# Kernel optimization log

Measured on AMD Instinct MI355X. Metric: run time of the kernel, lower is better.

The kernel has to match this reference:

```python
import jax, jax.numpy as jnp
import numpy as np

N, E, R = 50000, 1600000, 8
IN_F, HID_F, OUT_F = 128, 64, 64


def setup_inputs() -> dict:
    key = jax.random.key(0)
    ks = jax.random.split(key, 9)
    x = jax.random.normal(ks[0], (N, IN_F), dtype=jnp.float32)
    edge_index = jax.random.randint(ks[1], (2, E), 0, N, dtype=jnp.int64)
    edge_type = jax.random.randint(ks[2], (E,), 0, R, dtype=jnp.int64)
    # layer 1 params (scaled like glorot)
    s1 = 1.0 / np.sqrt(IN_F)
    W1_rel = jax.random.normal(ks[3], (R, IN_F, HID_F), dtype=jnp.float32) * s1
    W1_root = jax.random.normal(ks[4], (IN_F, HID_F), dtype=jnp.float32) * s1
    b1 = jnp.zeros((HID_F,), dtype=jnp.float32)
    # layer 2 params
    s2 = 1.0 / np.sqrt(HID_F)
    W2_rel = jax.random.normal(ks[5], (R, HID_F, OUT_F), dtype=jnp.float32) * s2
    W2_root = jax.random.normal(ks[6], (HID_F, OUT_F), dtype=jnp.float32) * s2
    b2 = jnp.zeros((OUT_F,), dtype=jnp.float32)
    return {"x": x, "edge_index": edge_index, "edge_type": edge_type,
            "W1_rel": W1_rel, "W1_root": W1_root, "b1": b1,
            "W2_rel": W2_rel, "W2_root": W2_root, "b2": b2}


def _rgcn_conv(x, src, dst, etype, W_rel, W_root, b):
    """PyG RGCNConv: root transform + per-relation mean-aggregated messages."""
    n = x.shape[0]
    r = W_rel.shape[0]
    # per-relation transform of all node features: [R, N, H]
    xw = jnp.einsum('nd,rdh->rnh', x, W_rel)
    # per-edge message: transformed source feature under the edge's relation
    msg = xw[etype, src]  # [E, H]
    # mean normalization per (dst, relation) pair
    key = dst * r + etype  # [E]
    cnt = jax.ops.segment_sum(jnp.ones(etype.shape, dtype=x.dtype), key,
                              num_segments=n * r)
    inv = 1.0 / jnp.maximum(cnt, 1.0)
    msg = msg * inv[key][:, None]
    # scatter-add into target nodes
    agg = jax.ops.segment_sum(msg, dst, num_segments=n)  # [N, H]
    return agg + x @ W_root + b


def reference(x, edge_index, edge_type, W1_rel, W1_root, b1, W2_rel, W2_root, b2):
    src, dst = edge_index[0], edge_index[1]
    h = _rgcn_conv(x, src, dst, edge_type, W1_rel, W1_root, b1)
    h = jax.nn.relu(h)
    out = _rgcn_conv(h, src, dst, edge_type, W2_rel, W2_root, b2)
    return out
```

## Files before the change

### kernel.cpp

```cpp
#include <hip/hip_runtime.h>


constexpr int NN  = 50000;
constexpr int NE  = 1600000;
constexpr int NR  = 8;
constexpr int FIN = 128;
constexpr int FH  = 64;

constexpr int BSH = 7;
constexpr int BN  = 1 << BSH;
constexpr int NB  = (NN + BN - 1) >> BSH;
constexpr int CAP = 6144;
constexpr int CH  = 4096;
constexpr int NAPP = (NE + CH - 1) / CH;

typedef __attribute__((ext_vector_type(8))) short bf16x8;
typedef __attribute__((ext_vector_type(4))) short bf16x4;
typedef __attribute__((ext_vector_type(4))) float f32x4;

__device__ __forceinline__ unsigned short f2bf(float f) {
  unsigned u = __float_as_uint(f);
  u = (u + 0x7fff + ((u >> 16) & 1)) >> 16;
  return (unsigned short)u;
}
__device__ __forceinline__ float bf2f(unsigned short b) {
  return __uint_as_float(((unsigned)b) << 16);
}
__device__ __forceinline__ bool edge_ok(unsigned s, unsigned d, unsigned r) {
  return s < NN && d < NN && r < NR;
}

__device__ void append_body(char* smem, int bx,
                            const int* __restrict__ src,
                            const int* __restrict__ dst,
                            const int* __restrict__ et,
                            int* __restrict__ bcur,
                            unsigned* __restrict__ brecs) {
  uint2* stage = (uint2*)smem;
  int* h     = (int*)(smem + (size_t)CH * 8);
  int* gbase = h + NB;
  int* sbase = gbase + NB;
  int* scur  = sbase + NB;
  int* wtot  = scur + NB;

  const int t  = threadIdx.x;
  const int c0 = bx * CH;
  const int m  = min(CH, NE - c0);

  for (int i = t; i < NB; i += 256) h[i] = 0;
  __syncthreads();

  for (int i = t; i < m; i += 256) {
    const unsigned s = (unsigned)src[c0 + i];
    const unsigned d = (unsigned)dst[c0 + i];
    const unsigned r = (unsigned)et[c0 + i];
    if (edge_ok(s, d, r)) atomicAdd(&h[d >> BSH], 1);
  }
  __syncthreads();

  const int v0 = (2 * t < NB) ? h[2 * t] : 0;
  const int v1 = (2 * t + 1 < NB) ? h[2 * t + 1] : 0;
  if (2 * t < NB     && v0) gbase[2 * t]     = atomicAdd(&bcur[2 * t], v0);
  if (2 * t + 1 < NB && v1) gbase[2 * t + 1] = atomicAdd(&bcur[2 * t + 1], v1);
  const int s = v0 + v1;
  int incl = s;
#pragma unroll
  for (int o = 1; o < 64; o <<= 1) {
    int u = __shfl_up(incl, o, 64);
    if ((t & 63) >= o) incl += u;
  }
  if ((t & 63) == 63) wtot[t >> 6] = incl;
  __syncthreads();
  int wo = 0;
  for (int w = 0; w < (t >> 6); ++w) wo += wtot[w];
  const int e = wo + incl - s;
  if (2 * t < NB)     { sbase[2 * t] = e;          scur[2 * t] = e; }
  if (2 * t + 1 < NB) { sbase[2 * t + 1] = e + v0; scur[2 * t + 1] = e + v0; }
  __syncthreads();

  for (int i = t; i < m; i += 256) {
    const unsigned sv = (unsigned)src[c0 + i];
    const unsigned d  = (unsigned)dst[c0 + i];
    const unsigned r  = (unsigned)et[c0 + i];
    if (edge_ok(sv, d, r)) {
      const int p = atomicAdd(&scur[d >> BSH], 1);
      if (p < CH) stage[p] = make_uint2((sv << 10) | (((unsigned)d & (BN - 1)) << 3) | r, d);
    }
  }
  __syncthreads();

  const int M = min(sbase[NB - 1] + h[NB - 1], CH);
  for (int j = t; j < M; j += 256) {
    const uint2 rec = stage[j];
    const int b = (int)(rec.y >> BSH);
    const int idx = min(gbase[b] + (j - sbase[b]), NB * CAP - 1);
    brecs[idx] = rec.x;
  }
}

__global__ void __launch_bounds__(256) bucket_finalize(
    const int* __restrict__ bcur, const unsigned* __restrict__ brecs,
    int* __restrict__ row_start, int* __restrict__ deg,
    unsigned* __restrict__ recs) {
  const int b    = blockIdx.x;
  const int base = b * CAP;
  const int m    = min(bcur[b] - base, CAP);
  const int d0   = b << BSH;
  __shared__ int cnt[BN * NR];
  __shared__ int curs[BN * NR];
  __shared__ int wtot[4];
  const int t = threadIdx.x;

  for (int i = t; i < BN * NR; i += 256) cnt[i] = 0;
  __syncthreads();
  for (int i = t; i < m; i += 256) {
    const unsigned rec = brecs[base + i];
    const int dl = (int)((rec >> 3) & (BN - 1));
    const int r  = (int)(rec & 7);
    atomicAdd(&cnt[dl * NR + r], 1);
  }
  __syncthreads();

  const int c0 = cnt[t * 4], c1 = cnt[t * 4 + 1], c2 = cnt[t * 4 + 2], c3 = cnt[t * 4 + 3];
  const int s = c0 + c1 + c2 + c3;
  int incl = s;
#pragma unroll
  for (int o = 1; o < 64; o <<= 1) {
    int u = __shfl_up(incl, o, 64);
    if ((t & 63) >= o) incl += u;
  }
  if ((t & 63) == 63) wtot[t >> 6] = incl;
  __syncthreads();
  int wo = 0;
  for (int w = 0; w < (t >> 6); ++w) wo += wtot[w];
  const int e = wo + incl - s;
  curs[t * 4]     = e;
  curs[t * 4 + 1] = e + c0;
  curs[t * 4 + 2] = e + c0 + c1;
  curs[t * 4 + 3] = e + c0 + c1 + c2;
  __syncthreads();

  if (t < BN) {
    const int d = d0 + t;
    if (d < NN) {
      const int start = curs[t * NR];
      const int end   = (t == BN - 1) ? m : curs[(t + 1) * NR];
      row_start[d] = base + start;
      deg[d]       = end - start;
    }
  }
  __syncthreads();

  for (int i = t; i < m; i += 256) {
    const unsigned rec = brecs[base + i];
    const int dl = (int)((rec >> 3) & (BN - 1));
    const int r  = (int)(rec & 7);
    const unsigned sv = rec >> 10;
    const int p  = atomicAdd(&curs[dl * NR + r], 1);
    const unsigned cn = (unsigned)min(cnt[dl * NR + r], 127);
    recs[base + min(p, CAP - 1)] = (cn << 25) | (((unsigned)r * NN + sv) << 6);
  }
}

__global__ void prep(const float* __restrict__ W1r, const float* __restrict__ W1o,
                     const float* __restrict__ W2r, const float* __restrict__ W2o,
                     unsigned short* __restrict__ Wt1,
                     unsigned short* __restrict__ Wt2,
                     int* __restrict__ bcur) {
  const int i  = blockIdx.x * blockDim.x + threadIdx.x;
  if (i < NB) bcur[i] = i * CAP;
  const int n1 = (NR + 1) * 64 * FIN;
  const int n2 = (NR + 1) * 64 * FH;
  if (i < n1) {
    const int g = i / (64 * FIN), rem = i % (64 * FIN);
    const int n = rem / FIN, k = rem % FIN;
    const float* W = (g < NR) ? (W1r + (size_t)g * FIN * 64) : W1o;
    Wt1[i] = f2bf(W[k * 64 + n]);
  } else if (i < n1 + n2) {
    const int j = i - n1;
    const int g = j / (64 * FH), rem = j % (64 * FH);
    const int n = rem / FH, k = rem % FH;
    const float* W = (g < NR) ? (W2r + (size_t)g * FH * 64) : W2o;
    Wt2[j] = f2bf(W[k * 64 + n]);
  }
}

template <int K, bool A_FP32, bool ROOT_BF16>
__device__ void gemm_body(char* smem, int bx,
                          const void* __restrict__ Av,
                          const unsigned short* __restrict__ Wt,
                          const float* __restrict__ bias,
                          unsigned short* __restrict__ xw,
                          void* __restrict__ root_out) {
  constexpr int KP  = K + 8;
  constexpr int NCH = 64 * (K / 8) / 256;
  constexpr int NKC = K / 32;
  unsigned short* Bs0 = (unsigned short*)smem;
  const int n0  = bx * 64;
  const int tid = threadIdx.x;
  const int wave = tid >> 6, lane = tid & 63;
  const int i16 = lane & 15, quad = lane >> 4;
  const int node = n0 + wave * 16 + i16;

  bf16x8 afrag[NKC];
  if constexpr (A_FP32) {
    const float* A = (const float*)Av;
#pragma unroll
    for (int kc = 0; kc < NKC; ++kc) {
      bf16x8 v = {};
      if (node < NN) {
        const float* p = A + (size_t)node * K + kc * 32 + quad * 8;
        const float4 f0 = *(const float4*)p;
        const float4 f1 = *(const float4*)(p + 4);
        v[0] = f2bf(f0.x); v[1] = f2bf(f0.y); v[2] = f2bf(f0.z); v[3] = f2bf(f0.w);
        v[4] = f2bf(f1.x); v[5] = f2bf(f1.y); v[6] = f2bf(f1.z); v[7] = f2bf(f1.w);
      }
      afrag[kc] = v;
    }
  } else {
    const unsigned short* A = (const unsigned short*)Av;
#pragma unroll
    for (int kc = 0; kc < NKC; ++kc) {
      bf16x8 v = {};
      if (node < NN) v = *(const bf16x8*)(A + (size_t)node * K + kc * 32 + quad * 8);
      afrag[kc] = v;
    }
  }

  for (int c = 0; c < NCH; ++c) {
    const int idx = tid + c * 256;
    const int row = idx / (K / 8), kp = (idx % (K / 8)) * 8;
    *(bf16x8*)(Bs0 + row * KP + kp) = *(const bf16x8*)(Wt + idx * 8);
  }
  __syncthreads();

  for (int g = 0; g <= NR; ++g) {
    const int buf = g & 1;
    unsigned short* Bc = Bs0 + buf * 64 * KP;
    unsigned short* Bn = Bs0 + (buf ^ 1) * 64 * KP;
    bf16x8 breg[NCH];
    if (g < NR) {
      const unsigned short* Wn = Wt + (size_t)(g + 1) * 64 * K;
#pragma unroll
      for (int c = 0; c < NCH; ++c) breg[c] = *(const bf16x8*)(Wn + (tid + c * 256) * 8);
    }

    f32x4 acc[4] = {};
#pragma unroll
    for (int kc = 0; kc < NKC; ++kc) {
      const int k0 = kc * 32 + quad * 8;
      const bf16x8 a0 = afrag[kc];
      const bf16x8 b0 = *(const bf16x8*)(Bc + (i16)      * KP + k0);
      const bf16x8 b1 = *(const bf16x8*)(Bc + (i16 + 16) * KP + k0);
      const bf16x8 b2 = *(const bf16x8*)(Bc + (i16 + 32) * KP + k0);
      const bf16x8 b3 = *(const bf16x8*)(Bc + (i16 + 48) * KP + k0);
      acc[0] = __builtin_amdgcn_mfma_f32_16x16x32_bf16(b0, a0, acc[0], 0, 0, 0);
      acc[1] = __builtin_amdgcn_mfma_f32_16x16x32_bf16(b1, a0, acc[1], 0, 0, 0);
      acc[2] = __builtin_amdgcn_mfma_f32_16x16x32_bf16(b2, a0, acc[2], 0, 0, 0);
      acc[3] = __builtin_amdgcn_mfma_f32_16x16x32_bf16(b3, a0, acc[3], 0, 0, 0);
    }

    if (g < NR) {
#pragma unroll
      for (int c = 0; c < NCH; ++c) {
        const int idx = tid + c * 256;
        const int row = idx / (K / 8), kp = (idx % (K / 8)) * 8;
        *(bf16x8*)(Bn + row * KP + kp) = breg[c];
      }
      if (node < NN) {
        unsigned short* p = xw + (size_t)g * (NN * 64) + (size_t)node * 64 + quad * 4;
#pragma unroll
        for (int ct = 0; ct < 4; ++ct) {
          bf16x4 ov;
          ov[0] = (short)f2bf(acc[ct][0]); ov[1] = (short)f2bf(acc[ct][1]);
          ov[2] = (short)f2bf(acc[ct][2]); ov[3] = (short)f2bf(acc[ct][3]);
          *(bf16x4*)(p + ct * 16) = ov;
        }
      }
    } else if (node < NN) {
#pragma unroll
      for (int ct = 0; ct < 4; ++ct) {
        const float4 bv = *(const float4*)(bias + ct * 16 + quad * 4);
        const float o0 = acc[ct][0] + bv.x, o1 = acc[ct][1] + bv.y;
        const float o2 = acc[ct][2] + bv.z, o3 = acc[ct][3] + bv.w;
        if constexpr (ROOT_BF16) {
          unsigned short* p = (unsigned short*)root_out + (size_t)node * 64 + ct * 16 + quad * 4;
          bf16x4 ov;
          ov[0] = (short)f2bf(o0); ov[1] = (short)f2bf(o1);
          ov[2] = (short)f2bf(o2); ov[3] = (short)f2bf(o3);
          *(bf16x4*)p = ov;
        } else {
          float* p = (float*)root_out + (size_t)node * 64 + ct * 16 + quad * 4;
          *(float4*)p = make_float4(o0, o1, o2, o3);
        }
      }
    }
    __syncthreads();
  }
}

__global__ void __launch_bounds__(256) fused_append_gemm1(
    const int* __restrict__ src, const int* __restrict__ dst,
    const int* __restrict__ et, int* __restrict__ bcur,
    unsigned* __restrict__ brecs,
    const float* __restrict__ A, const unsigned short* __restrict__ Wt,
    const float* __restrict__ bias, unsigned short* __restrict__ xw,
    unsigned short* __restrict__ hroot) {
  extern __shared__ char smem[];
  const int bx = (int)blockIdx.x;
  if (bx % 3 == 2 && bx / 3 < NAPP)
    append_body(smem, bx / 3, src, dst, et, bcur, brecs);
  else
    gemm_body<FIN, true, true>(smem, bx - (bx + 1) / 3, A, Wt, bias, xw, hroot);
}

__global__ void __launch_bounds__(256) gemm_l2(
    const unsigned short* __restrict__ A, const unsigned short* __restrict__ Wt,
    const float* __restrict__ bias, unsigned short* __restrict__ xw,
    float* __restrict__ out) {
  extern __shared__ char smem[];
  gemm_body<FH, false, false>(smem, (int)blockIdx.x, A, Wt, bias, xw, out);
}

template <bool RELU_BF16>
__global__ void __launch_bounds__(256) agg_csr(
    const int* __restrict__ row_start, const int* __restrict__ deg,
    const unsigned* __restrict__ recs, const unsigned short* __restrict__ xw,
    const void* __restrict__ rootv,
    float* __restrict__ out_f32, unsigned short* __restrict__ out_b16) {
  const int gid  = blockIdx.x * blockDim.x + threadIdx.x;
  const int lane = gid & 63;
  const int d    = gid >> 6;
  if (d >= NN) return;
  const int e  = lane >> 3;
  const int l8 = lane & 7;
  const int base = row_start[d];
  const int n    = deg[d];
  const unsigned* po = recs + base;
  const unsigned short* xp = xw + l8 * 8;
  float a[8] = {};

  int i0 = 0;
  for (; i0 + 32 < n; i0 += 64) {
    unsigned rr[8];
#pragma unroll
    for (int sl = 0; sl < 8; ++sl) {
      const int i = i0 + e + 8 * sl;
      rr[sl] = (i < n) ? po[i] : 0u;
    }
    bf16x8 vv[8];
#pragma unroll
    for (int sl = 0; sl < 8; ++sl)
      vv[sl] = *(const bf16x8*)(xp + (rr[sl] & 0x01FFFFFFu));
#pragma unroll
    for (int sl = 0; sl < 8; ++sl) {
      float w = __builtin_amdgcn_rcpf((float)(rr[sl] >> 25));
      if (i0 + e + 8 * sl >= n) w = 0.f;
#pragma unroll
      for (int q = 0; q < 8; ++q) a[q] += bf2f((unsigned short)vv[sl][q]) * w;
    }
  }
  if (i0 < n) {
    unsigned rr[4];
#pragma unroll
    for (int sl = 0; sl < 4; ++sl) {
      const int i = i0 + e + 8 * sl;
      rr[sl] = (i < n) ? po[i] : 0u;
    }
    bf16x8 vv[4];
#pragma unroll
    for (int sl = 0; sl < 4; ++sl)
      vv[sl] = *(const bf16x8*)(xp + (rr[sl] & 0x01FFFFFFu));
#pragma unroll
    for (int sl = 0; sl < 4; ++sl) {
      float w = __builtin_amdgcn_rcpf((float)(rr[sl] >> 25));
      if (i0 + e + 8 * sl >= n) w = 0.f;
#pragma unroll
      for (int q = 0; q < 8; ++q) a[q] += bf2f((unsigned short)vv[sl][q]) * w;
    }
  }

#pragma unroll
  for (int q = 0; q < 8; ++q) {
    a[q] += __shfl_xor(a[q], 8, 64);
    a[q] += __shfl_xor(a[q], 16, 64);
    a[q] += __shfl_xor(a[q], 32, 64);
  }

  if (e == 0) {
    float r[8];
    if constexpr (RELU_BF16) {
      const bf16x8 rv = *(const bf16x8*)((const unsigned short*)rootv + (size_t)d * 64 + l8 * 8);
#pragma unroll
      for (int q = 0; q < 8; ++q) r[q] = bf2f((unsigned short)rv[q]);
    } else {
      const float4 r0 = *(const float4*)((const float*)rootv + (size_t)d * 64 + l8 * 8);
      const float4 r1 = *(const float4*)((const float*)rootv + (size_t)d * 64 + l8 * 8 + 4);
      r[0] = r0.x; r[1] = r0.y; r[2] = r0.z; r[3] = r0.w;
      r[4] = r1.x; r[5] = r1.y; r[6] = r1.z; r[7] = r1.w;
    }
    float o[8];
#pragma unroll
    for (int q = 0; q < 8; ++q) o[q] = r[q] + a[q];
    if (RELU_BF16) {
      bf16x8 ov;
#pragma unroll
      for (int q = 0; q < 8; ++q) ov[q] = (short)f2bf(fmaxf(o[q], 0.f));
      *(bf16x8*)(out_b16 + (size_t)d * 64 + l8 * 8) = ov;
    } else {
      *(float4*)(out_f32 + (size_t)d * 64 + l8 * 8)     = make_float4(o[0], o[1], o[2], o[3]);
      *(float4*)(out_f32 + (size_t)d * 64 + l8 * 8 + 4) = make_float4(o[4], o[5], o[6], o[7]);
    }
  }
}

extern "C" void kernel_launch(void* const* d_in, const int* in_sizes, int n_in,
                              void* d_out, int out_size, void* d_ws, size_t ws_size,
                              hipStream_t stream) {
  const float* x   = (const float*)d_in[0];
  const int*   ei  = (const int*)d_in[1];
  const int*   et  = (const int*)d_in[2];
  const float* W1r = (const float*)d_in[3];
  const float* W1o = (const float*)d_in[4];
  const float* b1  = (const float*)d_in[5];
  const float* W2r = (const float*)d_in[6];
  const float* W2o = (const float*)d_in[7];
  const float* b2  = (const float*)d_in[8];
  float* out = (float*)d_out;

  const int* src = ei;
  const int* dst = ei + NE;

  char* ws = (char*)d_ws;
  size_t off = 0;
  auto alloc = [&](size_t bytes) {
    void* p = ws + off; off += (bytes + 255) & ~(size_t)255; return p;
  };
  int*   bcur      = (int*)alloc((size_t)NB * 4);
  int*   row_start = (int*)alloc((size_t)NN * 4);
  int*   deg       = (int*)alloc((size_t)NN * 4);
  unsigned* brecs  = (unsigned*)alloc((size_t)NB * CAP * 4);
  unsigned* offs   = (unsigned*)alloc((size_t)NB * CAP * 4);
  unsigned short* xw    = (unsigned short*)alloc((size_t)NN * NR * 64 * 2);
  unsigned short* hb    = (unsigned short*)alloc((size_t)NN * FH * 2);
  unsigned short* hroot = (unsigned short*)alloc((size_t)NN * 64 * 2);
  float*          root2 = (float*)alloc((size_t)NN * 64 * 4);
  unsigned short* Wt1   = (unsigned short*)alloc((size_t)(NR + 1) * 64 * FIN * 2);
  unsigned short* Wt2   = (unsigned short*)alloc((size_t)(NR + 1) * 64 * FH * 2);

  const int nprep = (NR + 1) * 64 * (FIN + FH);
  prep<<<(nprep + 255) / 256, 256, 0, stream>>>(W1r, W1o, W2r, W2o, Wt1, Wt2, bcur);

  const int gemm_blocks = (NN + 63) / 64;
  const int agg_blocks  = (NN * 64 + 255) / 256;
  constexpr int SM1 = CH * 8 + 4 * NB * 4 + 16;
  constexpr int SM2 = 2 * 64 * (FH + 8) * 2;

  fused_append_gemm1<<<NAPP + gemm_blocks, 256, SM1, stream>>>(
      src, dst, et, bcur, brecs, x, Wt1, b1, xw, hroot);
  bucket_finalize<<<NB, 256, 0, stream>>>(bcur, brecs, row_start, deg, offs);

  agg_csr<true><<<agg_blocks, 256, 0, stream>>>(row_start, deg, offs, xw, hroot, nullptr, hb);
  gemm_l2<<<gemm_blocks, 256, SM2, stream>>>(hb, Wt2, b2, xw, root2);
  agg_csr<false><<<agg_blocks, 256, 0, stream>>>(row_start, deg, offs, xw, root2, out, nullptr);
}
```

Measured before the change: 245.3 us.

## Cache edges in registers, shrink append chunks, single-buffer GEMM weight tiles

```diff
diff --git a/kernel.cpp b/kernel.cpp
--- a/kernel.cpp
+++ b/kernel.cpp
@@ -11,8 +11,9 @@
 constexpr int BN  = 1 << BSH;
 constexpr int NB  = (NN + BN - 1) >> BSH;
 constexpr int CAP = 6144;
-constexpr int CH  = 4096;
+constexpr int CH  = 2048;
 constexpr int NAPP = (NE + CH - 1) / CH;
+constexpr int APPLDS = CH * 8 + 4 * NB * 4 + 16;
 
 typedef __attribute__((ext_vector_type(8))) short bf16x8;
 typedef __attribute__((ext_vector_type(4))) short bf16x4;
@@ -48,14 +49,27 @@
   const int m  = min(CH, NE - c0);
 
   for (int i = t; i < NB; i += 256) h[i] = 0;
-  __syncthreads();
-
-  for (int i = t; i < m; i += 256) {
-    const unsigned s = (unsigned)src[c0 + i];
-    const unsigned d = (unsigned)dst[c0 + i];
-    const unsigned r = (unsigned)et[c0 + i];
-    if (edge_ok(s, d, r)) atomicAdd(&h[d >> BSH], 1);
-  }
+
+  unsigned rex[8], bux[8];
+#pragma unroll
+  for (int k = 0; k < 8; ++k) {
+    const int i = t + k * 256;
+    bux[k] = 0xFFFFFFFFu;
+    if (i < m) {
+      const unsigned sv = (unsigned)src[c0 + i];
+      const unsigned d  = (unsigned)dst[c0 + i];
+      const unsigned r  = (unsigned)et[c0 + i];
+      if (edge_ok(sv, d, r)) {
+        rex[k] = (sv << 10) | ((d & (BN - 1)) << 3) | r;
+        bux[k] = d >> BSH;
+      }
+    }
+  }
+  __syncthreads();
+
+#pragma unroll
+  for (int k = 0; k < 8; ++k)
+    if (bux[k] != 0xFFFFFFFFu) atomicAdd(&h[bux[k]], 1);
   __syncthreads();
 
   const int v0 = (2 * t < NB) ? h[2 * t] : 0;
@@ -78,13 +92,11 @@
   if (2 * t + 1 < NB) { sbase[2 * t + 1] = e + v0; scur[2 * t + 1] = e + v0; }
   __syncthreads();
 
-  for (int i = t; i < m; i += 256) {
-    const unsigned sv = (unsigned)src[c0 + i];
-    const unsigned d  = (unsigned)dst[c0 + i];
-    const unsigned r  = (unsigned)et[c0 + i];
-    if (edge_ok(sv, d, r)) {
-      const int p = atomicAdd(&scur[d >> BSH], 1);
-      if (p < CH) stage[p] = make_uint2((sv << 10) | (((unsigned)d & (BN - 1)) << 3) | r, d);
+#pragma unroll
+  for (int k = 0; k < 8; ++k) {
+    if (bux[k] != 0xFFFFFFFFu) {
+      const int p = atomicAdd(&scur[bux[k]], 1);
+      if (p < CH) stage[p] = make_uint2(rex[k], bux[k]);
     }
   }
   __syncthreads();
@@ -92,7 +104,7 @@
   const int M = min(sbase[NB - 1] + h[NB - 1], CH);
   for (int j = t; j < M; j += 256) {
     const uint2 rec = stage[j];
-    const int b = (int)(rec.y >> BSH);
+    const int b = (int)rec.y;
     const int idx = min(gbase[b] + (j - sbase[b]), NB * CAP - 1);
     brecs[idx] = rec.x;
   }
@@ -195,7 +207,7 @@
   constexpr int KP  = K + 8;
   constexpr int NCH = 64 * (K / 8) / 256;
   constexpr int NKC = K / 32;
-  unsigned short* Bs0 = (unsigned short*)smem;
+  unsigned short* Bs = (unsigned short*)smem;
   const int n0  = bx * 64;
   const int tid = threadIdx.x;
   const int wave = tid >> 6, lane = tid & 63;
@@ -230,14 +242,11 @@
   for (int c = 0; c < NCH; ++c) {
     const int idx = tid + c * 256;
     const int row = idx / (K / 8), kp = (idx % (K / 8)) * 8;
-    *(bf16x8*)(Bs0 + row * KP + kp) = *(const bf16x8*)(Wt + idx * 8);
+    *(bf16x8*)(Bs + row * KP + kp) = *(const bf16x8*)(Wt + idx * 8);
   }
   __syncthreads();
 
   for (int g = 0; g <= NR; ++g) {
-    const int buf = g & 1;
-    unsigned short* Bc = Bs0 + buf * 64 * KP;
-    unsigned short* Bn = Bs0 + (buf ^ 1) * 64 * KP;
     bf16x8 breg[NCH];
     if (g < NR) {
       const unsigned short* Wn = Wt + (size_t)(g + 1) * 64 * K;
@@ -250,10 +259,10 @@
     for (int kc = 0; kc < NKC; ++kc) {
       const int k0 = kc * 32 + quad * 8;
       const bf16x8 a0 = afrag[kc];
-      const bf16x8 b0 = *(const bf16x8*)(Bc + (i16)      * KP + k0);
-      const bf16x8 b1 = *(const bf16x8*)(Bc + (i16 + 16) * KP + k0);
-      const bf16x8 b2 = *(const bf16x8*)(Bc + (i16 + 32) * KP + k0);
-      const bf16x8 b3 = *(const bf16x8*)(Bc + (i16 + 48) * KP + k0);
+      const bf16x8 b0 = *(const bf16x8*)(Bs + (i16)      * KP + k0);
+      const bf16x8 b1 = *(const bf16x8*)(Bs + (i16 + 16) * KP + k0);
+      const bf16x8 b2 = *(const bf16x8*)(Bs + (i16 + 32) * KP + k0);
+      const bf16x8 b3 = *(const bf16x8*)(Bs + (i16 + 48) * KP + k0);
       acc[0] = __builtin_amdgcn_mfma_f32_16x16x32_bf16(b0, a0, acc[0], 0, 0, 0);
       acc[1] = __builtin_amdgcn_mfma_f32_16x16x32_bf16(b1, a0, acc[1], 0, 0, 0);
       acc[2] = __builtin_amdgcn_mfma_f32_16x16x32_bf16(b2, a0, acc[2], 0, 0, 0);
@@ -261,12 +270,6 @@
     }
 
     if (g < NR) {
-#pragma unroll
-      for (int c = 0; c < NCH; ++c) {
-        const int idx = tid + c * 256;
-        const int row = idx / (K / 8), kp = (idx % (K / 8)) * 8;
-        *(bf16x8*)(Bn + row * KP + kp) = breg[c];
-      }
       if (node < NN) {
         unsigned short* p = xw + (size_t)g * (NN * 64) + (size_t)node * 64 + quad * 4;
 #pragma unroll
@@ -277,6 +280,14 @@
           *(bf16x4*)(p + ct * 16) = ov;
         }
       }
+      __syncthreads();
+#pragma unroll
+      for (int c = 0; c < NCH; ++c) {
+        const int idx = tid + c * 256;
+        const int row = idx / (K / 8), kp = (idx % (K / 8)) * 8;
+        *(bf16x8*)(Bs + row * KP + kp) = breg[c];
+      }
+      __syncthreads();
     } else if (node < NN) {
 #pragma unroll
       for (int ct = 0; ct < 4; ++ct) {
@@ -295,7 +306,6 @@
         }
       }
     }
-    __syncthreads();
   }
 }
 
@@ -308,10 +318,10 @@
     unsigned short* __restrict__ hroot) {
   extern __shared__ char smem[];
   const int bx = (int)blockIdx.x;
-  if (bx % 3 == 2 && bx / 3 < NAPP)
-    append_body(smem, bx / 3, src, dst, et, bcur, brecs);
+  if (bx & 1)
+    append_body(smem, bx >> 1, src, dst, et, bcur, brecs);
   else
-    gemm_body<FIN, true, true>(smem, bx - (bx + 1) / 3, A, Wt, bias, xw, hroot);
+    gemm_body<FIN, true, true>(smem, bx >> 1, A, Wt, bias, xw, hroot);
 }
 
 __global__ void __launch_bounds__(256) gemm_l2(
@@ -453,8 +463,8 @@
 
   const int gemm_blocks = (NN + 63) / 64;
   const int agg_blocks  = (NN * 64 + 255) / 256;
-  constexpr int SM1 = CH * 8 + 4 * NB * 4 + 16;
-  constexpr int SM2 = 2 * 64 * (FH + 8) * 2;
+  constexpr int SM1 = APPLDS;
+  constexpr int SM2 = 64 * (FH + 8) * 2;
 
   fused_append_gemm1<<<NAPP + gemm_blocks, 256, SM1, stream>>>(
       src, dst, et, bcur, brecs, x, Wt1, b1, xw, hroot);
```

Result: slower. 251.9 us (+2.7%).
